# Kernel tuning notes

Measured on AMD Instinct MI355X. Metric: run time of the kernel, lower is better.

## Reference

```python
import jax, jax.numpy as jnp
import numpy as np

SQRT_2_OVER_PI = 0.79788456

def gelu_tanh(x):
    # tanh-approximate GELU, matches torch F.gelu(approximate='tanh')
    return 0.5 * x * (1.0 + jnp.tanh(SQRT_2_OVER_PI * x * (1.0 + 0.044715 * x * x)))

def gelu_bwd(x):
    # analytical derivative of tanh-approx GELU (same constants as source)
    t = jnp.tanh(SQRT_2_OVER_PI * x * (1.0 + 0.044715 * x * x))
    return 0.5 * x * ((1.0 - t * t) * (SQRT_2_OVER_PI + 0.1070322243 * x * x)) + 0.5 * (1.0 + t)

def setup_inputs() -> dict:
    key = jax.random.key(0)
    ks = jax.random.split(key, 6)
    T, d_phi, d_h = 8192, 4096, 64
    d_mid = 4 * d_h
    return {
        "phi_seq": jax.random.normal(ks[0], (T, d_phi), jnp.float32),
        "C_seq": jax.random.uniform(ks[1], (T,), jnp.float32),
        "theta_K_w": jax.random.normal(ks[2], (d_h, d_phi), jnp.float32) * 0.02,
        "theta_Q_w": jax.random.normal(ks[3], (d_h, d_phi), jnp.float32) * 0.02,
        "W10": jax.random.normal(ks[4], (d_h, d_mid), jnp.float32) * 0.02,
        "b10": jnp.zeros((d_mid,), jnp.float32),
        "W20": jax.random.normal(ks[5], (d_mid,), jnp.float32) * 0.02,
        "b20": jnp.zeros((), jnp.float32),
        "log_eta": jnp.asarray(np.log(0.01), jnp.float32),
    }

def reference(phi_seq, C_seq, theta_K_w, theta_Q_w, W10, b10, W20, b20, log_eta):
    eta = jnp.exp(log_eta)
    # Slow-weight projections hoisted out of the scan (same math, one big GEMM)
    u_Q = phi_seq @ theta_Q_w.T  # [T, d_h]
    u_K = phi_seq @ theta_K_w.T  # [T, d_h]

    def step(carry, inp):
        W1, b1, W2, b2 = carry
        u_q, u_k = inp
        # score with current fast weights
        s = jax.nn.sigmoid(gelu_tanh(u_q @ W1 + b1) @ W2 + b2)
        # update fast weights (inner objective, C_t = 0.0)
        Z1 = u_k @ W1 + b1          # [d_mid]
        X2 = gelu_tanh(Z1)
        pred = jax.nn.sigmoid(X2 @ W2 + b2)
        d_Z2 = 2.0 * pred * pred * (1.0 - pred)  # d/dZ2 of (pred-0)^2
        d_Z1 = (d_Z2 * W2) * gelu_bwd(Z1)
        new_carry = (
            W1 - eta * jnp.outer(u_k, d_Z1),
            b1 - eta * d_Z1,
            W2 - eta * d_Z2 * X2,
            b2 - eta * d_Z2,
        )
        return new_carry, s

    _, scores = jax.lax.scan(step, (W10, b10, W20, b20), (u_Q, u_K))
    outer_loss = jnp.sum((scores - C_seq) ** 2)
    return scores, outer_loss
```

## Files before the change

### kernel.cpp

```cpp
#include <hip/hip_runtime.h>
#include <hip/hip_bf16.h>

#define DH 64
#define DM 256

typedef float f32x2 __attribute__((ext_vector_type(2)));

__device__ __forceinline__ f32x2 sp2(float s) { return (f32x2){s, s}; }
__device__ __forceinline__ f32x2 pkfma(f32x2 a, f32x2 b, f32x2 c) {
#if __has_builtin(__builtin_elementwise_fma)
    return __builtin_elementwise_fma(a, b, c);
#else
    f32x2 r; r.x = fmaf(a.x, b.x, c.x); r.y = fmaf(a.y, b.y, c.y); return r;
#endif
}

__device__ __forceinline__ float tanh_fast(float y) {
    float e = __expf(2.0f * y);
    return 1.0f - 2.0f / (e + 1.0f);
}
__device__ __forceinline__ float sigmoid_fast(float x) {
    return 1.0f / (1.0f + __expf(-x));
}

template <int CTRL, int RMASK>
__device__ __forceinline__ float dpp_term(float x) {
    int p = __builtin_amdgcn_update_dpp(0, __float_as_int(x), CTRL, RMASK, 0xf, false);
    return __int_as_float(p);
}
__device__ __forceinline__ float wave_sum63(float x) {
    x += dpp_term<0xB1,  0xf>(x);
    x += dpp_term<0x4E,  0xf>(x);
    x += dpp_term<0x141, 0xf>(x);
    x += dpp_term<0x140, 0xf>(x);
    x += dpp_term<0x142, 0xa>(x);
    x += dpp_term<0x143, 0xc>(x);
    return x;
}

__global__ __launch_bounds__(256) void proj_kernel(
    const float* __restrict__ phi,
    const float* __restrict__ thK,
    const float* __restrict__ thQ,
    float* __restrict__ u,
    int dphi)
{
    const int tid  = threadIdx.x;
    const int th32 = tid & 31;
    const int tt8  = tid >> 5;
    const int t0   = tt8 * 4;
    const int h0   = th32 * 4;
    const int T0   = blockIdx.x * 32;

    __shared__ float sPhiT[32][36];
    __shared__ float sThT[32][128];

    const int h   = tid >> 1;
    const int ko  = (tid & 1) * 16;
    const float* trow = (h < 64) ? (thQ + (size_t)h * dphi)
                                 : (thK + (size_t)(h - 64) * dphi);
    const int tr  = tid >> 3;
    const int k4p = (tid & 7) * 4;

    float4 pv, tv0, tv1, tv2, tv3;
    pv  = *(const float4*)&phi[(size_t)(T0 + tr) * dphi + k4p];
    tv0 = *(const float4*)&trow[ko + 0];
    tv1 = *(const float4*)&trow[ko + 4];
    tv2 = *(const float4*)&trow[ko + 8];
    tv3 = *(const float4*)&trow[ko + 12];

    float acc[4][4];
    #pragma unroll
    for (int i = 0; i < 4; ++i)
        #pragma unroll
        for (int jj = 0; jj < 4; ++jj) acc[i][jj] = 0.0f;

    const int NC = dphi / 32;
    for (int c = 0; c < NC; ++c) {
        __syncthreads();
        sPhiT[k4p + 0][tr] = pv.x;
        sPhiT[k4p + 1][tr] = pv.y;
        sPhiT[k4p + 2][tr] = pv.z;
        sPhiT[k4p + 3][tr] = pv.w;
        sThT[ko +  0][h] = tv0.x;  sThT[ko +  1][h] = tv0.y;
        sThT[ko +  2][h] = tv0.z;  sThT[ko +  3][h] = tv0.w;
        sThT[ko +  4][h] = tv1.x;  sThT[ko +  5][h] = tv1.y;
        sThT[ko +  6][h] = tv1.z;  sThT[ko +  7][h] = tv1.w;
        sThT[ko +  8][h] = tv2.x;  sThT[ko +  9][h] = tv2.y;
        sThT[ko + 10][h] = tv2.z;  sThT[ko + 11][h] = tv2.w;
        sThT[ko + 12][h] = tv3.x;  sThT[ko + 13][h] = tv3.y;
        sThT[ko + 14][h] = tv3.z;  sThT[ko + 15][h] = tv3.w;
        __syncthreads();
        if (c + 1 < NC) {
            const int kb = (c + 1) * 32;
            pv  = *(const float4*)&phi[(size_t)(T0 + tr) * dphi + kb + k4p];
            tv0 = *(const float4*)&trow[kb + ko + 0];
            tv1 = *(const float4*)&trow[kb + ko + 4];
            tv2 = *(const float4*)&trow[kb + ko + 8];
            tv3 = *(const float4*)&trow[kb + ko + 12];
        }
        #pragma unroll 8
        for (int k = 0; k < 32; ++k) {
            float4 ph = *(const float4*)&sPhiT[k][t0];
            float4 th = *(const float4*)&sThT[k][h0];
            acc[0][0] = fmaf(ph.x, th.x, acc[0][0]);
            acc[0][1] = fmaf(ph.x, th.y, acc[0][1]);
            acc[0][2] = fmaf(ph.x, th.z, acc[0][2]);
            acc[0][3] = fmaf(ph.x, th.w, acc[0][3]);
            acc[1][0] = fmaf(ph.y, th.x, acc[1][0]);
            acc[1][1] = fmaf(ph.y, th.y, acc[1][1]);
            acc[1][2] = fmaf(ph.y, th.z, acc[1][2]);
            acc[1][3] = fmaf(ph.y, th.w, acc[1][3]);
            acc[2][0] = fmaf(ph.z, th.x, acc[2][0]);
            acc[2][1] = fmaf(ph.z, th.y, acc[2][1]);
            acc[2][2] = fmaf(ph.z, th.z, acc[2][2]);
            acc[2][3] = fmaf(ph.z, th.w, acc[2][3]);
            acc[3][0] = fmaf(ph.w, th.x, acc[3][0]);
            acc[3][1] = fmaf(ph.w, th.y, acc[3][1]);
            acc[3][2] = fmaf(ph.w, th.z, acc[3][2]);
            acc[3][3] = fmaf(ph.w, th.w, acc[3][3]);
        }
    }
    #pragma unroll
    for (int i = 0; i < 4; ++i) {
        float4 o;
        o.x = acc[i][0]; o.y = acc[i][1]; o.z = acc[i][2]; o.w = acc[i][3];
        *(float4*)&u[(size_t)(T0 + t0 + i) * 128 + h0] = o;
    }
}

__global__ __launch_bounds__(256) void dots2_kernel(
    const float* __restrict__ u, float2* __restrict__ dd2, int T)
{
    const int t    = (blockIdx.x * 256 + threadIdx.x) >> 6;
    const int lane = threadIdx.x & 63;
    if (t >= T) return;
    float ukt = u[(size_t)t * 128 + 64 + lane];
    float k1 = (t >= 1) ? u[(size_t)(t - 1) * 128 + 64 + lane] : 0.f;
    float k2 = (t >= 2) ? u[(size_t)(t - 2) * 128 + 64 + lane] : 0.f;
    float p1 = k1 * ukt, p2 = k2 * ukt;
    #pragma unroll
    for (int off = 32; off > 0; off >>= 1) {
        p1 += __shfl_xor(p1, off);
        p2 += __shfl_xor(p2, off);
    }
    if (lane == 0) dd2[t] = make_float2(p1, p2);
}

__global__ __launch_bounds__(256, 1) void scan_k4(
    const float* __restrict__ u,
    const float2* __restrict__ dd2g,
    const float* __restrict__ W10,
    const float* __restrict__ b10,
    const float* __restrict__ W20,
    const float* __restrict__ b20,
    const float* __restrict__ log_eta,
    float* __restrict__ e1s,
    float* __restrict__ g2s,
    float* __restrict__ dz2s,
    float* __restrict__ snapW,
    float* __restrict__ snapB1,
    float* __restrict__ snapW2,
    float* __restrict__ snapB2,
    int T)
{
    const int j    = threadIdx.x;
    const int lane = j & 63;
    const int wv   = j >> 6;
    const int uko  = 16 * wv;

    __shared__ __align__(16) float  ubuf[2][64][68];
    __shared__ __align__(16) float  pbuf[2][4][256];
    __shared__ __align__(16) float  ebufT[4][4][72];
    __shared__ __align__(16) float  pqk[2][4];
    __shared__ __align__(16) float2 dbuf[2][64];

    const int NB = T >> 6;
    const int sl = j >> 2, qq = j & 3;

    {
        const float* src = u + (size_t)sl * 128 + 64 + qq * 16;
        #pragma unroll
        for (int k = 0; k < 4; ++k)
            *(float4*)&ubuf[0][sl][qq * 16 + k * 4] = *(const float4*)&src[k * 4];
        if (j < 64) dbuf[0][j] = dd2g[j];
        if (j < 4)  pqk[1][j] = -2.5e29f;
        float* ez = &ebufT[2][0][0];
        for (int k = j; k < 2 * 4 * 72; k += 256) ez[k] = 0.f;
    }

    f32x2 w1p[32];
    #pragma unroll
    for (int i = 0; i < 16; ++i) {
        float4 wr = *(const float4*)&W10[(uko + i) * DM + lane * 4];
        w1p[2 * i]     = (f32x2){wr.x, wr.y};
        w1p[2 * i + 1] = (f32x2){wr.z, wr.w};
    }
    float b1j = b10[j];
    float w2j = W20[j];
    float b2  = b20[0];
    const float eta = __expf(log_eta[0]);
    float dZ2p = 0.f, en1 = 0.f, en2 = 0.f, x2p = 0.f;

    __syncthreads();

    {
        const float* ur0 = &ubuf[0][0][uko];
        f32x2 a0 = sp2(0.f), a1 = sp2(0.f);
        #pragma unroll
        for (int q = 0; q < 4; ++q) {
            float4 us = *(const float4*)&ur0[q * 4];
            a0 = pkfma(sp2(us.x), w1p[8*q+0], a0); a1 = pkfma(sp2(us.x), w1p[8*q+1], a1);
            a0 = pkfma(sp2(us.y), w1p[8*q+2], a0); a1 = pkfma(sp2(us.y), w1p[8*q+3], a1);
            a0 = pkfma(sp2(us.z), w1p[8*q+4], a0); a1 = pkfma(sp2(us.z), w1p[8*q+5], a1);
            a0 = pkfma(sp2(us.w), w1p[8*q+6], a0); a1 = pkfma(sp2(us.w), w1p[8*q+7], a1);
        }
        float4 wk; wk.x = a0.x; wk.y = a0.y; wk.z = a1.x; wk.w = a1.y;
        *(float4*)&pbuf[0][wv][lane * 4] = wk;
    }
    __syncthreads();

    float4 st[4];
    float2 std2 = make_float2(0.f, 0.f);

    for (int t = 0; t < T; ++t) {
        const int r   = t & 63;
        const int B   = t >> 6;
        const int bs  = B & 1;
        const int pbR = t & 1;

        float4 pqK = *(const float4*)&pqk[pbR ^ 1][0];
        const int sE = (t + 2) & 3;
        float eb0 = ebufT[sE][0][lane];
        float eb1 = ebufT[sE][1][lane];
        float eb2 = ebufT[sE][2][lane];
        float eb3 = ebufT[sE][3][lane];
        float2 dd = dbuf[bs][r];
        float pB0 = pbuf[pbR][0][j], pB1 = pbuf[pbR][1][j];
        float pB2 = pbuf[pbR][2][j], pB3 = pbuf[pbR][3][j];
        const int rn = (t + 1 < T) ? t + 1 : T - 1;
        const int rm = (t >= 2) ? t - 2 : 0;
        const float* urN = &ubuf[(rn >> 6) & 1][rn & 63][uko];
        const float* urM = &ubuf[(rm >> 6) & 1][rm & 63][uko];
        float4 n0 = *(const float4*)&urN[0],  n1 = *(const float4*)&urN[4];
        float4 n2 = *(const float4*)&urN[8],  n3 = *(const float4*)&urN[12];
        float4 m0 = *(const float4*)&urM[0],  m1 = *(const float4*)&urM[4];
        float4 m2 = *(const float4*)&urM[8],  m3 = *(const float4*)&urM[12];

        float zp   = ((pqK.x + pqK.y) + (pqK.z + pqK.w)) + b2;
        float pred = sigmoid_fast(zp);
        float dZ2  = 2.f * pred * pred * (1.f - pred);
        float e1o  = dZ2 * en1;
        if (t > 0) {
            e1s[(size_t)(t - 1) * 256 + j] = e1o;
            g2s[(size_t)(t - 1) * 256 + j] = dZ2 * x2p;
            if (j == 0) dz2s[t - 1] = dZ2;
        }

        f32x2 e1g0 = sp2(dZ2p) * (f32x2){eb0, eb1};
        f32x2 e1g1 = sp2(dZ2p) * (f32x2){eb2, eb3};
        f32x2 a0 = sp2(0.f), a1 = sp2(0.f);
#define ROWK(ib, ums, uns) {                                   \
        f32x2 wa = pkfma(sp2(-(ums)), e1g0, w1p[ib]);          \
        f32x2 wb = pkfma(sp2(-(ums)), e1g1, w1p[(ib) + 1]);    \
        w1p[ib] = wa; w1p[(ib) + 1] = wb;                      \
        a0 = pkfma(sp2(uns), wa, a0);                          \
        a1 = pkfma(sp2(uns), wb, a1); }
        ROWK(0,  m0.x, n0.x); ROWK(2,  m0.y, n0.y);
        ROWK(4,  m0.z, n0.z); ROWK(6,  m0.w, n0.w);
        ROWK(8,  m1.x, n1.x); ROWK(10, m1.y, n1.y);
        ROWK(12, m1.z, n1.z); ROWK(14, m1.w, n1.w);
        ROWK(16, m2.x, n2.x); ROWK(18, m2.y, n2.y);
        ROWK(20, m2.z, n2.z); ROWK(22, m2.w, n2.w);
        ROWK(24, m3.x, n3.x); ROWK(26, m3.y, n3.y);
        ROWK(28, m3.z, n3.z); ROWK(30, m3.w, n3.w);
#undef ROWK
        { float4 wk; wk.x = a0.x; wk.y = a0.y; wk.z = a1.x; wk.w = a1.y;
          *(float4*)&pbuf[pbR ^ 1][wv][lane * 4] = wk; }

        if ((t & 127) == 1) {
            float* dW = snapW + (size_t)(t >> 7) * 16384;
            #pragma unroll
            for (int i = 0; i < 16; ++i) {
                float4 wr;
                wr.x = w1p[2 * i].x;     wr.y = w1p[2 * i].y;
                wr.z = w1p[2 * i + 1].x; wr.w = w1p[2 * i + 1].y;
                *(float4*)&dW[(uko + i) * 256 + lane * 4] = wr;
            }
        }

        float e1o2 = dZ2p * en2;
        b1j -= e1o;
        w2j  = fmaf(-eta * dZ2, x2p, w2j);
        b2  -= eta * dZ2;

        if ((t & 127) == 0) {
            const int cs_ = t >> 7;
            snapB1[cs_ * 256 + j] = b1j;
            snapW2[cs_ * 256 + j] = w2j;
            if (j == 0) snapB2[cs_] = b2;
        }

        float Pk = ((pB0 + pB1) + (pB2 + pB3));
        float zk = Pk + b1j - e1o2 * dd.y - e1o * dd.x;
        float tk = tanh_fast(0.79788456f * zk * fmaf(0.044715f, zk * zk, 1.f));
        float x2 = 0.5f * zk * (1.f + tk);
        float gb = 0.5f * zk * ((1.f - tk * tk) *
                   fmaf(0.1070322243f, zk * zk, 0.79788456f))
                 + 0.5f * (1.f + tk);
        float en = eta * w2j * gb;
        ebufT[t & 3][j & 3][j >> 2] = en;
        float pk = wave_sum63(x2 * w2j);
        if (lane == 63) pqk[t & 1][wv] = pk;

        dZ2p = dZ2; en2 = en1; en1 = en; x2p = x2;

        if (r == 0 && B + 1 < NB) {
            const float* src = u + (size_t)((B + 1) * 64 + sl) * 128 + 64 + qq * 16;
            #pragma unroll
            for (int k = 0; k < 4; ++k) st[k] = *(const float4*)&src[k * 4];
            if (j < 64) std2 = dd2g[(B + 1) * 64 + j];
        }
        if (r == 32 && B + 1 < NB) {
            #pragma unroll
            for (int k = 0; k < 4; ++k)
                *(float4*)&ubuf[bs ^ 1][sl][qq * 16 + k * 4] = st[k];
            if (j < 64) dbuf[bs ^ 1][j] = std2;
        }

        asm volatile("s_waitcnt lgkmcnt(0)" ::: "memory");
        __builtin_amdgcn_s_barrier();
        asm volatile("" ::: "memory");
    }

    {
        float4 pqK = *(const float4*)&pqk[(T - 1) & 1][0];
        float zp   = ((pqK.x + pqK.y) + (pqK.z + pqK.w)) + b2;
        float pred = sigmoid_fast(zp);
        float dZ2  = 2.f * pred * pred * (1.f - pred);
        e1s[(size_t)(T - 1) * 256 + j] = dZ2 * en1;
        g2s[(size_t)(T - 1) * 256 + j] = dZ2 * x2p;
        if (j == 0) dz2s[T - 1] = dZ2;
    }
}

#define TB 32
__global__ __launch_bounds__(256) void scores_kernel(
    const float* __restrict__ u,
    const float* __restrict__ e1s,
    const float* __restrict__ g2s,
    const float* __restrict__ dz2s,
    const float* __restrict__ snapW,
    const float* __restrict__ snapB1,
    const float* __restrict__ snapW2,
    const float* __restrict__ snapB2,
    const float* __restrict__ log_eta,
    float* __restrict__ out,
    int T)
{
    const int tid = threadIdx.x;
    const int t0  = blockIdx.x * TB;
    const int j   = tid;
    const int wv  = tid >> 6;
    const int lane = tid & 63;
    const int snapc = t0 >> 7;

    __shared__ __align__(16) float uq[TB][68];
    __shared__ __align__(16) float uk[TB][68];
    __shared__ __align__(16) float Dl[TB][36];
    __shared__ float redl[2][4];

    #pragma unroll
    for (int k = 0; k < 2; ++k) {
        int idx = tid * 2 + k;
        int tl = idx >> 4, c4 = idx & 15;
        *(float4*)&uq[tl][c4 * 4] = *(const float4*)&u[(size_t)(t0 + tl) * 128 + c4 * 4];
    }
    const float eta = __expf(log_eta[0]);
    float w2p = snapW2[snapc * 256 + j];
    float b2p = snapB2[snapc];
    float b1j = snapB1[snapc * 256 + j];
    __syncthreads();

    float acc[TB];
    {
        const float* Wsn = snapW + (size_t)snapc * 16384;
        float wcol[64];
        #pragma unroll
        for (int i = 0; i < 64; ++i) wcol[i] = Wsn[i * DM + j];
        for (int tl = 0; tl < TB; ++tl) {
            float a = b1j;
            #pragma unroll
            for (int q = 0; q < 16; ++q) {
                float4 uv = *(const float4*)&uq[tl][q * 4];
                a = fmaf(uv.x, wcol[4*q+0], a);
                a = fmaf(uv.y, wcol[4*q+1], a);
                a = fmaf(uv.z, wcol[4*q+2], a);
                a = fmaf(uv.w, wcol[4*q+3], a);
            }
            acc[tl] = a;
        }
    }

    const int cs = snapc << 2;
    const int ce = t0 >> 5;
    for (int c = cs; c <= ce; ++c) {
        const int sc = c * TB;
        __syncthreads();
        #pragma unroll
        for (int k = 0; k < 2; ++k) {
            int idx = tid * 2 + k;
            int sl = idx >> 4, c4 = idx & 15;
            *(float4*)&uk[sl][c4 * 4] = *(const float4*)&u[(size_t)(sc + sl) * 128 + 64 + c4 * 4];
        }
        __syncthreads();
        {
            int tl = tid & 31, sg = tid >> 5;
            float4 uqr[16];
            #pragma unroll
            for (int q = 0; q < 16; ++q) uqr[q] = *(const float4*)&uq[tl][q * 4];
            #pragma unroll
            for (int k = 0; k < 4; ++k) {
                int sl = sg * 4 + k;
                float d = 0.f;
                #pragma unroll
                for (int q = 0; q < 16; ++q) {
                    float4 ukr = *(const float4*)&uk[sl][q * 4];
                    d = fmaf(ukr.x, uqr[q].x, d);
                    d = fmaf(ukr.y, uqr[q].y, d);
                    d = fmaf(ukr.z, uqr[q].z, d);
                    d = fmaf(ukr.w, uqr[q].w, d);
                }
                Dl[sl][tl] = d;
            }
        }
        __syncthreads();

        const bool lastc = (c == ce);
        if (!lastc) {
            float e1acc = 0.f;
            for (int sl = 0; sl < TB; ++sl) {
                const int s = sc + sl;
                float e1v = e1s[(size_t)s * 256 + j];
                float g2v = g2s[(size_t)s * 256 + j];
                float dzv = dz2s[s];
                w2p = fmaf(-eta, g2v, w2p);
                b2p = fmaf(-eta, dzv, b2p);
                e1acc += e1v;
                float4 dreg[8];
                #pragma unroll
                for (int q = 0; q < 8; ++q) dreg[q] = *(const float4*)&Dl[sl][q * 4];
                #pragma unroll
                for (int tl = 0; tl < TB; ++tl) {
                    float D = (tl & 2) ? ((tl & 1) ? dreg[tl>>2].w : dreg[tl>>2].z)
                                       : ((tl & 1) ? dreg[tl>>2].y : dreg[tl>>2].x);
                    acc[tl] = fmaf(-e1v, D, acc[tl]);
                }
            }
            #pragma unroll
            for (int tl = 0; tl < TB; ++tl) acc[tl] -= e1acc;
        } else {
            for (int sl = 0; sl < TB; ++sl) {
                const int s = sc + sl;
                float zq = 0.f;
                #pragma unroll
                for (int tl = 0; tl < TB; ++tl) if (tl == sl) zq = acc[tl];
                float tq = tanh_fast(0.79788456f * zq * fmaf(0.044715f, zq*zq, 1.f));
                float aq = 0.5f * zq * (1.f + tq);
                float v  = wave_sum63(aq * w2p);
                if (lane == 63) redl[sl & 1][wv] = v;
                __syncthreads();
                float zs = redl[sl & 1][0] + redl[sl & 1][1] + redl[sl & 1][2] + redl[sl & 1][3] + b2p;
                if (tid == 0) out[t0 + sl] = sigmoid_fast(zs);

                float e1v = e1s[(size_t)s * 256 + j];
                float g2v = g2s[(size_t)s * 256 + j];
                float dzv = dz2s[s];
                w2p = fmaf(-eta, g2v, w2p);
                b2p = fmaf(-eta, dzv, b2p);
                float4 dreg[8];
                #pragma unroll
                for (int q = 0; q < 8; ++q) dreg[q] = *(const float4*)&Dl[sl][q * 4];
                #pragma unroll
                for (int tl = 0; tl < TB; ++tl) {
                    float D = (tl & 2) ? ((tl & 1) ? dreg[tl>>2].w : dreg[tl>>2].z)
                                       : ((tl & 1) ? dreg[tl>>2].y : dreg[tl>>2].x);
                    float e1m = (tl > sl) ? e1v : 0.f;
                    acc[tl] = fmaf(-e1m, D + 1.f, acc[tl]);
                }
            }
        }
    }
}

__global__ __launch_bounds__(256) void loss_kernel(
    const float* __restrict__ C, float* __restrict__ out, int T)
{
    const int tid = threadIdx.x;
    const int wv = tid >> 6, lane = tid & 63;
    __shared__ float part[4];
    float acc = 0.f;
    for (int t = tid; t < T; t += 256) {
        float d = out[t] - C[t];
        acc = fmaf(d, d, acc);
    }
    acc = wave_sum63(acc);
    if (lane == 63) part[wv] = acc;
    __syncthreads();
    if (tid == 0) out[T] = ((part[0] + part[1]) + (part[2] + part[3]));
}

extern "C" void kernel_launch(void* const* d_in, const int* in_sizes, int n_in,
                              void* d_out, int out_size, void* d_ws, size_t ws_size,
                              hipStream_t stream) {
    const float* phi     = (const float*)d_in[0];
    const float* C_seq   = (const float*)d_in[1];
    const float* thK     = (const float*)d_in[2];
    const float* thQ     = (const float*)d_in[3];
    const float* W10     = (const float*)d_in[4];
    const float* b10     = (const float*)d_in[5];
    const float* W20     = (const float*)d_in[6];
    const float* b20     = (const float*)d_in[7];
    const float* log_eta = (const float*)d_in[8];

    const int T    = in_sizes[1];
    const int dphi = in_sizes[0] / T;
    const int NS   = T >> 7;

    char* ws = (char*)d_ws;
    size_t off = 0;
    float*  uw     = (float*)(ws + off);  off += (size_t)T * 128 * 4;
    float2* dd2    = (float2*)(ws + off); off += (size_t)T * 2 * 4;
    float*  dz2s   = (float*)(ws + off);  off += (size_t)T * 4;
    float*  e1s    = (float*)(ws + off);  off += (size_t)T * 256 * 4;
    float*  g2s    = (float*)(ws + off);  off += (size_t)T * 256 * 4;
    float*  snapW  = (float*)(ws + off);  off += (size_t)NS * 16384 * 4;
    float*  snapB1 = (float*)(ws + off);  off += (size_t)NS * 256 * 4;
    float*  snapW2 = (float*)(ws + off);  off += (size_t)NS * 256 * 4;
    float*  snapB2 = (float*)(ws + off);  off += (size_t)NS * 4;

    proj_kernel<<<T / 32, 256, 0, stream>>>(phi, thK, thQ, uw, dphi);
    dots2_kernel<<<T / 4, 256, 0, stream>>>(uw, dd2, T);
    scan_k4<<<1, 256, 0, stream>>>(uw, dd2, W10, b10, W20, b20, log_eta,
                                   e1s, g2s, dz2s,
                                   snapW, snapB1, snapW2, snapB2, T);
    scores_kernel<<<T / TB, 256, 0, stream>>>(uw, e1s, g2s, dz2s,
                                              snapW, snapB1, snapW2, snapB2,
                                              log_eta, (float*)d_out, T);
    loss_kernel<<<1, 256, 0, stream>>>(C_seq, (float*)d_out, T);
}
```

Baseline: 5.808 ms.

## Rebuild weight snapshots in parallel kernels instead of inside the serial scan

Removes the periodic snapshot stores of W1, b1, W2 and b2 from the single-block serial scan. Two new kernels rebuild the snapshots afterwards from the stored per-step update vectors. One computes each 128-step chunk's accumulated weight delta in parallel, and the other runs a prefix subtraction across chunks starting from the initial weights. This shortens the serial critical path at the cost of two extra launches, re-reading e1s/g2s, and possible floating-point differences from reassociating the updates.

```diff
diff --git a/kernel.cpp b/kernel.cpp
--- a/kernel.cpp
+++ b/kernel.cpp
@@ -158,10 +158,6 @@
     float* __restrict__ e1s,
     float* __restrict__ g2s,
     float* __restrict__ dz2s,
-    float* __restrict__ snapW,
-    float* __restrict__ snapB1,
-    float* __restrict__ snapW2,
-    float* __restrict__ snapB2,
     int T)
 {
     const int j    = threadIdx.x;
@@ -278,29 +274,10 @@
         { float4 wk; wk.x = a0.x; wk.y = a0.y; wk.z = a1.x; wk.w = a1.y;
           *(float4*)&pbuf[pbR ^ 1][wv][lane * 4] = wk; }
 
-        if ((t & 127) == 1) {
-            float* dW = snapW + (size_t)(t >> 7) * 16384;
-            #pragma unroll
-            for (int i = 0; i < 16; ++i) {
-                float4 wr;
-                wr.x = w1p[2 * i].x;     wr.y = w1p[2 * i].y;
-                wr.z = w1p[2 * i + 1].x; wr.w = w1p[2 * i + 1].y;
-                *(float4*)&dW[(uko + i) * 256 + lane * 4] = wr;
-            }
-        }
-
         float e1o2 = dZ2p * en2;
         b1j -= e1o;
         w2j  = fmaf(-eta * dZ2, x2p, w2j);
         b2  -= eta * dZ2;
-
-        if ((t & 127) == 0) {
-            const int cs_ = t >> 7;
-            snapB1[cs_ * 256 + j] = b1j;
-            snapW2[cs_ * 256 + j] = w2j;
-            if (j == 0) snapB2[cs_] = b2;
-        }
-
         float Pk = ((pB0 + pB1) + (pB2 + pB3));
         float zk = Pk + b1j - e1o2 * dd.y - e1o * dd.x;
         float tk = tanh_fast(0.79788456f * zk * fmaf(0.044715f, zk * zk, 1.f));
@@ -341,6 +318,106 @@
         e1s[(size_t)(T - 1) * 256 + j] = dZ2 * en1;
         g2s[(size_t)(T - 1) * 256 + j] = dZ2 * x2p;
         if (j == 0) dz2s[T - 1] = dZ2;
+    }
+}
+
+__global__ __launch_bounds__(256) void delta_kernel(
+    const float* __restrict__ u,
+    const float* __restrict__ e1s,
+    const float* __restrict__ g2s,
+    const float* __restrict__ dz2s,
+    float* __restrict__ snapW,
+    float* __restrict__ snapB1,
+    float* __restrict__ snapW2,
+    float* __restrict__ snapB2)
+{
+    const int b  = blockIdx.x + 1;
+    const int s0 = (b - 1) * 128;
+    const int j  = threadIdx.x;
+
+    __shared__ __align__(16) float uks[128][64];
+
+    #pragma unroll
+    for (int k = 0; k < 8; ++k) {
+        int l = k * 256 + j;
+        int s = l >> 4, q = l & 15;
+        *(float4*)&uks[s][q * 4] =
+            *(const float4*)&u[(size_t)(s0 + s) * 128 + 64 + q * 4];
+    }
+    __syncthreads();
+
+    float acc[64];
+    #pragma unroll
+    for (int i = 0; i < 64; ++i) acc[i] = 0.f;
+    float sB1 = 0.f, sW2 = 0.f, sB2 = 0.f;
+
+    for (int s = 0; s < 128; ++s) {
+        float e1v = e1s[(size_t)(s0 + s) * 256 + j];
+        float g2v = g2s[(size_t)(s0 + s) * 256 + j];
+        sB1 += e1v;
+        sW2 += g2v;
+        sB2 += dz2s[s0 + s];
+        #pragma unroll
+        for (int q = 0; q < 16; ++q) {
+            float4 uv = *(const float4*)&uks[s][q * 4];
+            acc[4*q+0] = fmaf(uv.x, e1v, acc[4*q+0]);
+            acc[4*q+1] = fmaf(uv.y, e1v, acc[4*q+1]);
+            acc[4*q+2] = fmaf(uv.z, e1v, acc[4*q+2]);
+            acc[4*q+3] = fmaf(uv.w, e1v, acc[4*q+3]);
+        }
+    }
+
+    float* dW = snapW + (size_t)b * 16384;
+    #pragma unroll
+    for (int i = 0; i < 64; ++i) dW[i * 256 + j] = acc[i];
+    snapB1[b * 256 + j] = sB1;
+    snapW2[b * 256 + j] = sW2;
+    if (j == 0) snapB2[b] = sB2;
+}
+
+__global__ __launch_bounds__(256) void prefix_kernel(
+    const float* __restrict__ W10,
+    const float* __restrict__ b10,
+    const float* __restrict__ W20,
+    const float* __restrict__ b20,
+    const float* __restrict__ log_eta,
+    float* __restrict__ snapW,
+    float* __restrict__ snapB1,
+    float* __restrict__ snapW2,
+    float* __restrict__ snapB2,
+    int NS)
+{
+    const int i = blockIdx.x;
+    const int j = threadIdx.x;
+    const float eta = __expf(log_eta[0]);
+
+    float w = W10[i * 256 + j];
+    snapW[(size_t)0 * 16384 + i * 256 + j] = w;
+    for (int c = 1; c < NS; ++c) {
+        float d = snapW[(size_t)c * 16384 + i * 256 + j];
+        w -= d;
+        snapW[(size_t)c * 16384 + i * 256 + j] = w;
+    }
+
+    if (i == 0) {
+        float b1 = b10[j];
+        float w2 = W20[j];
+        snapB1[j] = b1;
+        snapW2[j] = w2;
+        for (int c = 1; c < NS; ++c) {
+            b1 -= snapB1[c * 256 + j];
+            w2 -= eta * snapW2[c * 256 + j];
+            snapB1[c * 256 + j] = b1;
+            snapW2[c * 256 + j] = w2;
+        }
+        if (j == 0) {
+            float b2 = b20[0];
+            snapB2[0] = b2;
+            for (int c = 1; c < NS; ++c) {
+                b2 -= eta * snapB2[c];
+                snapB2[c] = b2;
+            }
+        }
     }
 }
 
@@ -542,8 +619,11 @@
     proj_kernel<<<T / 32, 256, 0, stream>>>(phi, thK, thQ, uw, dphi);
     dots2_kernel<<<T / 4, 256, 0, stream>>>(uw, dd2, T);
     scan_k4<<<1, 256, 0, stream>>>(uw, dd2, W10, b10, W20, b20, log_eta,
-                                   e1s, g2s, dz2s,
-                                   snapW, snapB1, snapW2, snapB2, T);
+                                   e1s, g2s, dz2s, T);
+    delta_kernel<<<NS - 1, 256, 0, stream>>>(uw, e1s, g2s, dz2s,
+                                             snapW, snapB1, snapW2, snapB2);
+    prefix_kernel<<<64, 256, 0, stream>>>(W10, b10, W20, b20, log_eta,
+                                          snapW, snapB1, snapW2, snapB2, NS);
     scores_kernel<<<T / TB, 256, 0, stream>>>(uw, e1s, g2s, dz2s,
                                               snapW, snapB1, snapW2, snapB2,
                                               log_eta, (float*)d_out, T);
```

New measurement: 5.450 ms (median of 3 runs). 1.07x faster.
